# Kernel optimization log

Measured on AMD Instinct MI355X. Metric: run time of the kernel, lower is better.

The kernel has to match this reference:

```python
import jax, jax.numpy as jnp
import numpy as np

HEADS = 8
DH = 64          # value head dim == kernel head dim (expansion ratio 1.0)
DIM = 256
BOT = 256        # bottleneck_dim
DOUT = 256
HID = 4 * 256    # MLP hidden (expansion_ratio=4)
EPS_LN = 1e-5
EPS_GN = 1e-6


def layer_norm(x, g, b):
    m = x.mean(axis=-1, keepdims=True)
    v = x.var(axis=-1, keepdims=True)
    return (x - m) / jnp.sqrt(v + EPS_LN) * g + b


def rotate_half(x):
    x1, x2 = jnp.split(x, 2, axis=-1)
    return jnp.concatenate([-x2, x1], axis=-1)


def apply_rope(t, cos, sin):
    return t * cos + rotate_half(t) * sin


def mlp(x, W1, b1, W2, b2):
    return jax.nn.gelu(x @ W1 + b1) @ W2 + b2


def pooling_reducer(x, Win, W1, b1, W2, b2):
    # x: (b, n, m, c); mean-pool over axis 2, then MLP
    x = x @ Win
    x = x.mean(axis=2)
    return mlp(x, W1, b1, W2, b2)


def dp_kernel(x, Wqk, cos, sin):
    # x: (b, n, BOT) -> softmax attention kernel (b, h, n, n)
    b, n, _ = x.shape
    qk = (x @ Wqk).reshape(b, n, 2, HEADS, DH).transpose(0, 3, 2, 1, 4)  # b h 2 n d
    qk = apply_rope(qk, cos, sin)
    q, k = qk[:, :, 0], qk[:, :, 1]
    attn = jnp.einsum('bhid,bhjd->bhij', q, k) * (1.0 / DH)  # softmax scale = 1/dim_head
    return jax.nn.softmax(attn, axis=-1)


def group_norm(x):
    # channels-last GroupNorm(heads groups, affine=False), per position
    b, i, l, _ = x.shape
    xg = x.reshape(b, i, l, HEADS, DH)
    m = xg.mean(axis=-1, keepdims=True)
    v = xg.var(axis=-1, keepdims=True)
    return ((xg - m) / jnp.sqrt(v + EPS_GN)).reshape(b, i, l, HEADS * DH)


def setup_inputs() -> dict:
    key = jax.random.key(0)
    ks = jax.random.split(key, 32)
    B, NY, NX = 4, 128, 128
    s = 0.02
    d = {
        'u': jax.random.normal(ks[0], (B, NY, NX, DIM), jnp.float32),
        'rotary_cos_y': jax.random.uniform(ks[1], (NY, DH), jnp.float32),
        'rotary_sin_y': jax.random.uniform(ks[2], (NY, DH), jnp.float32),
        'rotary_cos_x': jax.random.uniform(ks[3], (NX, DH), jnp.float32),
        'rotary_sin_x': jax.random.uniform(ks[4], (NX, DH), jnp.float32),
        'scalar_cond': jax.random.normal(ks[5], (B,), jnp.float32),
        # norms
        'ln1_g': jnp.ones((DIM,), jnp.float32), 'ln1_b': jnp.zeros((DIM,), jnp.float32),
        'ln2_g': jnp.ones((DIM,), jnp.float32), 'ln2_b': jnp.zeros((DIM,), jnp.float32),
        # to_v
        'Wv': jax.random.normal(ks[6], (DIM, HEADS * DH), jnp.float32) * s,
        # to_y PoolingReducer
        'Wy_in': jax.random.normal(ks[7], (DIM, DIM), jnp.float32) * s,
        'Wy1': jax.random.normal(ks[8], (DIM, HID), jnp.float32) * s,
        'by1': jnp.zeros((HID,), jnp.float32),
        'Wy2': jax.random.normal(ks[9], (HID, BOT), jnp.float32) * s,
        'by2': jnp.zeros((BOT,), jnp.float32),
        # to_x PoolingReducer
        'Wx_in': jax.random.normal(ks[10], (DIM, DIM), jnp.float32) * s,
        'Wx1': jax.random.normal(ks[11], (DIM, HID), jnp.float32) * s,
        'bx1': jnp.zeros((HID,), jnp.float32),
        'Wx2': jax.random.normal(ks[12], (HID, BOT), jnp.float32) * s,
        'bx2': jnp.zeros((BOT,), jnp.float32),
        # kernels
        'Wqk_x': jax.random.normal(ks[13], (BOT, 2 * HEADS * DH), jnp.float32) * s,
        'Wqk_y': jax.random.normal(ks[14], (BOT, 2 * HEADS * DH), jnp.float32) * s,
        # merge head
        'Wm': jax.random.normal(ks[15], (HEADS * DH, DOUT), jnp.float32) * s,
        'bm': jnp.zeros((DOUT,), jnp.float32),
        # ffn
        'Wf1': jax.random.normal(ks[16], (DOUT, 4 * DOUT), jnp.float32) * s,
        'bf1': jnp.zeros((4 * DOUT,), jnp.float32),
        'Wf2': jax.random.normal(ks[17], (4 * DOUT, DOUT), jnp.float32) * s,
        'bf2': jnp.zeros((DOUT,), jnp.float32),
    }
    return d


def reference(u, rotary_cos_y, rotary_sin_y, rotary_cos_x, rotary_sin_x, scalar_cond,
              ln1_g, ln1_b, ln2_g, ln2_b, Wv,
              Wy_in, Wy1, by1, Wy2, by2,
              Wx_in, Wx1, bx1, Wx2, bx2,
              Wqk_x, Wqk_y, Wm, bm, Wf1, bf1, Wf2, bf2):
    b, ny, nx, _ = u.shape
    u_skip = u
    un = layer_norm(u, ln1_g, ln1_b)
    # to_x: transpose grid then pool over (now) second spatial axis -> (b, nx, BOT)
    u_x = pooling_reducer(un.transpose(0, 2, 1, 3), Wx_in, Wx1, bx1, Wx2, bx2)
    # to_y: pool over nx -> (b, ny, BOT)
    u_y = pooling_reducer(un, Wy_in, Wy1, by1, Wy2, by2)
    k_x = dp_kernel(u_x, Wqk_x, rotary_cos_x, rotary_sin_x)  # (b,h,nx,nx)
    k_y = dp_kernel(u_y, Wqk_y, rotary_cos_y, rotary_sin_y)  # (b,h,ny,ny)
    # values: b i l (h c) -> b h i l c
    v = (un @ Wv).reshape(b, ny, nx, HEADS, DH).transpose(0, 3, 1, 2, 4)
    u_phi = jnp.einsum('bhij,bhjmc->bhimc', k_y, v)
    u_phi = jnp.einsum('bhlm,bhimc->bhilc', k_x, u_phi)
    u_phi = u_phi.transpose(0, 2, 3, 1, 4).reshape(b, ny, nx, HEADS * DH)
    u2 = group_norm(u_phi) @ Wm + bm + u_skip  # dropout is identity in eval
    out = mlp(layer_norm(u2, ln2_g, ln2_b), Wf1, bf1, Wf2, bf2) + u2
    return out
```

## Files before the change

### kernel.cpp

```cpp
#include <hip/hip_runtime.h>
#include <hip/hip_bf16.h>
#include <math.h>

#define NB 4
#define NY 128
#define NX 128
#define DIM 256
#define NH 8
#define DH_ 64
#define HDIM 512
#define HID 1024
#define NPOS (NB*NY*NX)

typedef __hip_bfloat16 bf16_t;
typedef __attribute__((ext_vector_type(8))) short short8;
typedef __attribute__((ext_vector_type(4))) float f32x4;

__device__ __forceinline__ float b2f(bf16_t x){ return __bfloat162float(x); }
__device__ __forceinline__ bf16_t f2b(float x){ return __float2bfloat16(x); }
__device__ __forceinline__ short f2s(float x){ bf16_t h = __float2bfloat16(x); return *reinterpret_cast<short*>(&h); }
__device__ __forceinline__ float s2f(short x){ bf16_t h = *reinterpret_cast<bf16_t*>(&x); return __bfloat162float(h); }


__device__ __forceinline__ float gelu_tanh(float x){
  float z = 1.5957691216057308f*(x + 0.044715f*x*x*x);
  return x / (1.0f + __expf(-z));
}

__global__ void __launch_bounds__(256) k_pack(const float* __restrict__ W,
    short* __restrict__ out, int K, int N){
  int tid = blockIdx.x*256 + threadIdx.x;
  int lane = tid & 63;
  int rem = tid >> 6;
  int ntiles = N >> 4;
  int nt = rem % ntiles, kb = rem / ntiles;
  int n = nt*16 + (lane & 15);
  int k0 = kb*32 + (lane>>4)*8;
  short8 v;
  #pragma unroll
  for (int j=0;j<8;j++) v[j] = f2s(W[(size_t)(k0+j)*N + n]);
  *(short8*)&out[(size_t)tid*8] = v;
}

__global__ void __launch_bounds__(256) k_ln1(const float* __restrict__ u,
    const float* __restrict__ g, const float* __restrict__ b,
    bf16_t* __restrict__ un){
  int wave = threadIdx.x >> 6, lane = threadIdx.x & 63;
  size_t row = (size_t)blockIdx.x*4 + wave;
  const float* x = u + row*DIM;
  float v[4]; float s=0.f, ss=0.f;
  #pragma unroll
  for (int j=0;j<4;j++){ float t = x[lane + j*64]; v[j]=t; s+=t; ss+=t*t; }
  #pragma unroll
  for (int off=32;off>0;off>>=1){ s += __shfl_down(s,off,64); ss += __shfl_down(ss,off,64); }
  s = __shfl(s,0,64); ss = __shfl(ss,0,64);
  float m = s*(1.0f/DIM);
  float var = ss*(1.0f/DIM) - m*m;
  float r = rsqrtf(var + 1e-5f);
  bf16_t* o = un + row*DIM;
  #pragma unroll
  for (int j=0;j<4;j++){
    int f = lane + j*64;
    o[f] = f2b((v[j]-m)*r*g[f] + b[f]);
  }
}

__global__ void __launch_bounds__(256) k_pool_y(const bf16_t* __restrict__ un, float* __restrict__ pooly){
  int by = blockIdx.x;
  int d = threadIdx.x;
  size_t base = (size_t)by*NX*DIM + d;
  float s = 0.f;
  for (int x=0;x<NX;x++) s += b2f(un[base + (size_t)x*DIM]);
  pooly[(size_t)by*DIM + d] = s*(1.0f/NX);
}
__global__ void __launch_bounds__(256) k_pool_x(const bf16_t* __restrict__ un, float* __restrict__ poolx){
  int bb = blockIdx.x / NX, x = blockIdx.x % NX;
  int d = threadIdx.x;
  size_t base = ((size_t)bb*NY*NX + x)*DIM + d;
  float s = 0.f;
  for (int y=0;y<NY;y++) s += b2f(un[base + (size_t)y*NX*DIM]);
  poolx[(size_t)blockIdx.x*DIM + d] = s*(1.0f/NY);
}

#define GS_STRIDE 72
__global__ void __launch_bounds__(256) k_gemm_mfma(const float* __restrict__ A,
    const short* __restrict__ WP, const float* __restrict__ bias,
    float* __restrict__ C, int N, int K, int dogelu){
  __shared__ __align__(16) short As[64*GS_STRIDE];
  int tid = threadIdx.x;
  int lane = tid & 63, w = tid >> 6;
  int am = lane & 15, aq = lane >> 4;
  int m0 = blockIdx.x*64;
  int nt0 = blockIdx.y*16;
  int ntiles = N >> 4;
  f32x4 o[4][4];
  #pragma unroll
  for (int mt=0;mt<4;mt++)
    #pragma unroll
    for (int nt=0;nt<4;nt++) o[mt][nt] = (f32x4){0.f,0.f,0.f,0.f};

  for (int kc=0; kc<K; kc+=64){
    #pragma unroll
    for (int it=0; it<4; it++){
      int q = tid + it*256;
      int r = q >> 4, c4 = q & 15;
      float4 v = *(const float4*)&A[(size_t)(m0+r)*K + kc + c4*4];
      ushort4 p;
      p.x = (ushort)f2s(v.x); p.y = (ushort)f2s(v.y);
      p.z = (ushort)f2s(v.z); p.w = (ushort)f2s(v.w);
      *(ushort4*)&As[r*GS_STRIDE + c4*4] = p;
    }
    __syncthreads();
    #pragma unroll
    for (int kb=0; kb<2; kb++){
      short8 a[4], bfr[4];
      #pragma unroll
      for (int mt=0;mt<4;mt++)
        a[mt] = *(const short8*)&As[(mt*16+am)*GS_STRIDE + kb*32 + aq*8];
      int kbg = (kc>>5) + kb;
      #pragma unroll
      for (int nt=0;nt<4;nt++){
        int ntg = nt0 + w*4 + nt;
        bfr[nt] = *(const short8*)&WP[(size_t)((kbg*ntiles + ntg)*64 + lane)*8];
      }
      #pragma unroll
      for (int mt=0;mt<4;mt++)
        #pragma unroll
        for (int nt=0;nt<4;nt++)
          o[mt][nt] = __builtin_amdgcn_mfma_f32_16x16x32_bf16(a[mt], bfr[nt], o[mt][nt], 0,0,0);
    }
    __syncthreads();
  }

  #pragma unroll
  for (int nt=0;nt<4;nt++){
    int col = (nt0 + w*4 + nt)*16 + am;
    float bv = bias ? bias[col] : 0.f;
    #pragma unroll
    for (int mt=0;mt<4;mt++){
      #pragma unroll
      for (int reg=0;reg<4;reg++){
        int row = m0 + mt*16 + aq*4 + reg;
        float val = o[mt][nt][reg] + bv;
        if (dogelu) val = gelu_tanh(val);
        C[(size_t)row*N + col] = val;
      }
    }
  }
}

__global__ void __launch_bounds__(256) k_rope(const float* __restrict__ qk,
    const float* __restrict__ cs, const float* __restrict__ sn,
    float* __restrict__ q, float* __restrict__ k){
  int idx = blockIdx.x*256 + threadIdx.x;
  int c = idx & 63;
  int h = (idx>>6) & 7;
  int p = (idx>>9) & 1;
  int n = (idx>>10) & 127;
  int bb = idx>>17;
  float t = qk[idx];
  float t2 = qk[(c<32) ? idx+32 : idx-32];
  if (c<32) t2 = -t2;
  float val = t*cs[n*64+c] + t2*sn[n*64+c];
  float* dst = p ? k : q;
  dst[(((size_t)bb*NH + h)*128 + n)*64 + c] = val;
}

__global__ void __launch_bounds__(128) k_attn(const float* __restrict__ q,
    const float* __restrict__ k, bf16_t* __restrict__ attn){
  int i = blockIdx.x & 127;
  int bh = blockIdx.x >> 7;
  __shared__ float qs[64];
  __shared__ float sm[128];
  int tid = threadIdx.x;
  const float* qrow = q + ((size_t)bh*128 + i)*64;
  if (tid < 64) qs[tid] = qrow[tid];
  __syncthreads();
  const float* krow = k + ((size_t)bh*128 + tid)*64;
  float dot = 0.f;
  for (int c=0;c<64;c++) dot += qs[c]*krow[c];
  dot *= (1.0f/64.0f);
  sm[tid] = dot;
  __syncthreads();
  float mx = -1e30f;
  for (int j=0;j<128;j++) mx = fmaxf(mx, sm[j]);
  __syncthreads();
  float e = expf(dot - mx);
  sm[tid] = e;
  __syncthreads();
  float s = 0.f;
  for (int j=0;j<128;j++) s += sm[j];
  attn[(size_t)blockIdx.x*128 + tid] = f2b(e/s);
}

#define AST 136
#define UST 72
#define VST 136
__global__ void __launch_bounds__(256) k_phi1m(const bf16_t* __restrict__ un,
    const short* __restrict__ WvP, const bf16_t* __restrict__ attn,
    bf16_t* __restrict__ phi){
  int m  = blockIdx.x & (NX-1);
  int bh = blockIdx.x >> 7;
  int b  = bh >> 3, h = bh & 7;
  __shared__ __align__(16) short At[128*AST];
  __shared__ __align__(16) short unc[128*UST];
  __shared__ __align__(16) short Vt[64*VST];
  int tid = threadIdx.x;
  int lane = tid & 63, w = tid >> 6;
  int am = lane & 15, aq = lane >> 4;

  {
    const ushort* ag = (const ushort*)attn + (size_t)bh*16384;
    #pragma unroll
    for (int it=0; it<16; it++){
      int q = tid + it*256;
      int i = q >> 5, j4 = q & 31;
      *(ushort4*)&At[i*AST + j4*4] = *(const ushort4*)(ag + i*128 + j4*4);
    }
  }

  f32x4 v[2][4];
  #pragma unroll
  for (int mt=0;mt<2;mt++)
    #pragma unroll
    for (int nt=0;nt<4;nt++) v[mt][nt] = (f32x4){0.f,0.f,0.f,0.f};
  const ushort* ug = (const ushort*)un;
  for (int kc=0; kc<4; kc++){
    #pragma unroll
    for (int it=0; it<8; it++){
      int q = tid + it*256;
      int y = q >> 4, c4 = q & 15;
      *(ushort4*)&unc[y*UST + c4*4] =
          *(const ushort4*)(ug + (((size_t)b*NY + y)*NX + m)*DIM + kc*64 + c4*4);
    }
    __syncthreads();
    #pragma unroll
    for (int kb=0; kb<2; kb++){
      short8 a2[2], bb[4];
      #pragma unroll
      for (int mt=0;mt<2;mt++)
        a2[mt] = *(const short8*)&unc[(w*32 + mt*16 + am)*UST + kb*32 + aq*8];
      int kbg = kc*2 + kb;
      #pragma unroll
      for (int nt=0;nt<4;nt++)
        bb[nt] = *(const short8*)&WvP[(size_t)((kbg*32 + (h*4+nt))*64 + lane)*8];
      #pragma unroll
      for (int mt=0;mt<2;mt++)
        #pragma unroll
        for (int nt=0;nt<4;nt++)
          v[mt][nt] = __builtin_amdgcn_mfma_f32_16x16x32_bf16(a2[mt], bb[nt], v[mt][nt], 0,0,0);
    }
    __syncthreads();
  }
  #pragma unroll
  for (int mt=0;mt<2;mt++)
    #pragma unroll
    for (int nt=0;nt<4;nt++){
      int c = nt*16 + am;
      int y0 = w*32 + mt*16 + aq*4;
      ushort4 pk;
      pk.x = (ushort)f2s(v[mt][nt][0]);
      pk.y = (ushort)f2s(v[mt][nt][1]);
      pk.z = (ushort)f2s(v[mt][nt][2]);
      pk.w = (ushort)f2s(v[mt][nt][3]);
      *(ushort4*)&Vt[c*VST + y0] = pk;
    }
  __syncthreads();

  f32x4 o[2][4];
  #pragma unroll
  for (int mt=0;mt<2;mt++)
    #pragma unroll
    for (int nt=0;nt<4;nt++) o[mt][nt] = (f32x4){0.f,0.f,0.f,0.f};
  #pragma unroll
  for (int kb=0; kb<4; kb++){
    short8 a2[2], bb[4];
    #pragma unroll
    for (int mt=0;mt<2;mt++)
      a2[mt] = *(const short8*)&At[(w*32 + mt*16 + am)*AST + kb*32 + aq*8];
    #pragma unroll
    for (int nt=0;nt<4;nt++)
      bb[nt] = *(const short8*)&Vt[(nt*16 + am)*VST + kb*32 + aq*8];
    #pragma unroll
    for (int mt=0;mt<2;mt++)
      #pragma unroll
      for (int nt=0;nt<4;nt++)
        o[mt][nt] = __builtin_amdgcn_mfma_f32_16x16x32_bf16(a2[mt], bb[nt], o[mt][nt], 0,0,0);
  }
  ushort* pg = (ushort*)phi + (size_t)bh*NY*NX*DH_ + (size_t)m*DH_;
  #pragma unroll
  for (int mt=0;mt<2;mt++)
    #pragma unroll
    for (int nt=0;nt<4;nt++)
      #pragma unroll
      for (int reg=0;reg<4;reg++){
        int i = w*32 + mt*16 + aq*4 + reg;
        int c = nt*16 + am;
        pg[(size_t)i*(NX*DH_) + c] = (ushort)f2s(o[mt][nt][reg]);
      }
}

__global__ void __launch_bounds__(256) k_phi2m(const bf16_t* __restrict__ attn,
    bf16_t* __restrict__ phi){
  int i  = blockIdx.x & (NY-1);
  int bh = blockIdx.x >> 7;
  __shared__ __align__(16) short Ax[128*AST];
  __shared__ __align__(16) short Pt[64*VST];
  int tid = threadIdx.x;
  int lane = tid & 63, w = tid >> 6;
  int am = lane & 15, aq = lane >> 4;

  {
    const ushort* ag = (const ushort*)attn + (size_t)bh*16384;
    #pragma unroll
    for (int it=0; it<16; it++){
      int q = tid + it*256;
      int r = q >> 5, j4 = q & 31;
      *(ushort4*)&Ax[r*AST + j4*4] = *(const ushort4*)(ag + r*128 + j4*4);
    }
  }
  ushort* pg = (ushort*)phi + (size_t)(bh*NY + i)*(NX*DH_);
  #pragma unroll
  for (int it=0; it<8; it++){
    int q = tid + it*256;
    int mm = q >> 4, c4 = q & 15;
    ushort4 v4 = *(const ushort4*)(pg + mm*DH_ + c4*4);
    Pt[(c4*4+0)*VST + mm] = v4.x;
    Pt[(c4*4+1)*VST + mm] = v4.y;
    Pt[(c4*4+2)*VST + mm] = v4.z;
    Pt[(c4*4+3)*VST + mm] = v4.w;
  }
  __syncthreads();

  f32x4 o[2][4];
  #pragma unroll
  for (int mt=0;mt<2;mt++)
    #pragma unroll
    for (int nt=0;nt<4;nt++) o[mt][nt] = (f32x4){0.f,0.f,0.f,0.f};
  #pragma unroll
  for (int kb=0; kb<4; kb++){
    short8 a2[2], bb[4];
    #pragma unroll
    for (int mt=0;mt<2;mt++)
      a2[mt] = *(const short8*)&Ax[(w*32 + mt*16 + am)*AST + kb*32 + aq*8];
    #pragma unroll
    for (int nt=0;nt<4;nt++)
      bb[nt] = *(const short8*)&Pt[(nt*16 + am)*VST + kb*32 + aq*8];
    #pragma unroll
    for (int mt=0;mt<2;mt++)
      #pragma unroll
      for (int nt=0;nt<4;nt++)
        o[mt][nt] = __builtin_amdgcn_mfma_f32_16x16x32_bf16(a2[mt], bb[nt], o[mt][nt], 0,0,0);
  }
  #pragma unroll
  for (int mt=0;mt<2;mt++)
    #pragma unroll
    for (int nt=0;nt<4;nt++)
      #pragma unroll
      for (int reg=0;reg<4;reg++){
        int l = w*32 + mt*16 + aq*4 + reg;
        int c = nt*16 + am;
        pg[(size_t)l*DH_ + c] = (ushort)f2s(o[mt][nt][reg]);
      }
}

#define GN_STRIDE 520
__global__ void __launch_bounds__(512) k_gn_wm(const bf16_t* __restrict__ phi,
    const short* __restrict__ WmP, const float* __restrict__ bm,
    const float* __restrict__ u, float* __restrict__ u2){
  __shared__ __align__(16) short X[64*GN_STRIDE];
  __shared__ float mean_s[512], rstd_s[512];
  int tid = threadIdx.x;
  int lane = tid & 63, w = tid >> 6;
  int wh = w >> 2, wl = w & 3;
  size_t p0 = (size_t)blockIdx.x*64;
  int b  = (int)(p0 >> 14);
  int y  = (int)((p0 >> 7) & 127);
  int x0 = (int)(p0 & 127);

  #pragma unroll
  for (int it=0; it<16; it++){
    int q = tid + it*512;
    int r = q >> 7, f4 = q & 127;
    int h = f4 >> 4, c4 = f4 & 15;
    const ushort* src = (const ushort*)phi +
        ((((size_t)b*NH + h)*NY + y)*NX + (x0 + r))*DH_ + c4*4;
    *(ushort4*)&X[r*GN_STRIDE + f4*4] = *(const ushort4*)src;
  }
  __syncthreads();
  {
    int g = tid;
    int r = g >> 3, h = g & 7;
    const short* base = &X[r*GN_STRIDE + h*64];
    float s=0.f, ss=0.f;
    #pragma unroll
    for (int i=0;i<16;i++){
      ushort4 v4 = *(const ushort4*)&base[i*4];
      float a = s2f((short)v4.x), bq = s2f((short)v4.y), cq = s2f((short)v4.z), d = s2f((short)v4.w);
      s += a+bq+cq+d; ss += a*a+bq*bq+cq*cq+d*d;
    }
    float mm = s*(1.0f/64.0f);
    float vv = ss*(1.0f/64.0f) - mm*mm;
    mean_s[g] = mm;
    rstd_s[g] = rsqrtf(vv + 1e-6f);
  }
  __syncthreads();
  #pragma unroll
  for (int it=0; it<16; it++){
    int q = tid + it*512;
    int r = q >> 7, f4 = q & 127;
    int h = f4 >> 4;
    float mm = mean_s[r*8 + h], rs = rstd_s[r*8 + h];
    short* ptr = &X[r*GN_STRIDE + f4*4];
    ushort4 v4 = *(ushort4*)ptr;
    v4.x = (ushort)f2s((s2f((short)v4.x)-mm)*rs);
    v4.y = (ushort)f2s((s2f((short)v4.y)-mm)*rs);
    v4.z = (ushort)f2s((s2f((short)v4.z)-mm)*rs);
    v4.w = (ushort)f2s((s2f((short)v4.w)-mm)*rs);
    *(ushort4*)ptr = v4;
  }
  __syncthreads();

  f32x4 o[2][4];
  #pragma unroll
  for (int mt=0;mt<2;mt++)
    #pragma unroll
    for (int nt=0;nt<4;nt++) o[mt][nt] = (f32x4){0.f,0.f,0.f,0.f};
  int am = lane & 15, aq = lane >> 4;
  for (int kb=0; kb<16; kb++){
    short8 a[2], bfr[4];
    #pragma unroll
    for (int mt=0;mt<2;mt++)
      a[mt] = *(const short8*)&X[(wh*32 + mt*16 + am)*GN_STRIDE + kb*32 + aq*8];
    #pragma unroll
    for (int nt=0;nt<4;nt++)
      bfr[nt] = *(const short8*)&WmP[(size_t)((kb*16 + (wl*4+nt))*64 + lane)*8];
    #pragma unroll
    for (int mt=0;mt<2;mt++)
      #pragma unroll
      for (int nt=0;nt<4;nt++)
        o[mt][nt] = __builtin_amdgcn_mfma_f32_16x16x32_bf16(a[mt], bfr[nt], o[mt][nt], 0,0,0);
  }
  #pragma unroll
  for (int nt=0;nt<4;nt++){
    int col = wl*64 + nt*16 + am;
    float bmv = bm[col];
    #pragma unroll
    for (int mt=0;mt<2;mt++){
      #pragma unroll
      for (int reg=0;reg<4;reg++){
        size_t p = p0 + wh*32 + mt*16 + aq*4 + reg;
        u2[p*DIM + col] = o[mt][nt][reg] + bmv + u[p*DIM + col];
      }
    }
  }
}

#define ML_STRIDE 264
__global__ void __launch_bounds__(512) k_mlp_out(float* u2,
    const float* __restrict__ g2, const float* __restrict__ b2,
    const short* __restrict__ Wf1P, const float* __restrict__ bf1,
    const short* __restrict__ Wf2P, const float* __restrict__ bf2){
  __shared__ __align__(16) short X[64*ML_STRIDE];
  __shared__ __align__(16) short H[64*ML_STRIDE];
  int tid = threadIdx.x;
  int lane = tid & 63, w = tid >> 6;
  int wh = w >> 2, wl = w & 3;
  size_t p0 = (size_t)blockIdx.x*64;

  float4 g4 = *(const float4*)&g2[lane*4];
  float4 bq4 = *(const float4*)&b2[lane*4];
  for (int rr=0; rr<8; rr++){
    int r = w*8 + rr;
    float4 v = *(const float4*)&u2[(p0 + r)*DIM + lane*4];
    float s = v.x+v.y+v.z+v.w;
    float ss = v.x*v.x+v.y*v.y+v.z*v.z+v.w*v.w;
    #pragma unroll
    for (int off=32;off>0;off>>=1){ s += __shfl_down(s,off,64); ss += __shfl_down(ss,off,64); }
    s = __shfl(s,0,64); ss = __shfl(ss,0,64);
    float m = s*(1.0f/DIM);
    float rstd = rsqrtf(ss*(1.0f/DIM) - m*m + 1e-5f);
    ushort4 xo;
    xo.x = (ushort)f2s((v.x-m)*rstd*g4.x + bq4.x);
    xo.y = (ushort)f2s((v.y-m)*rstd*g4.y + bq4.y);
    xo.z = (ushort)f2s((v.z-m)*rstd*g4.z + bq4.z);
    xo.w = (ushort)f2s((v.w-m)*rstd*g4.w + bq4.w);
    *(ushort4*)&X[r*ML_STRIDE + lane*4] = xo;
  }
  __syncthreads();

  int am = lane & 15, aq = lane >> 4;
  f32x4 o[2][4];
  #pragma unroll
  for (int mt=0;mt<2;mt++)
    #pragma unroll
    for (int nt=0;nt<4;nt++) o[mt][nt] = (f32x4){0.f,0.f,0.f,0.f};

  for (int nc=0; nc<4; nc++){
    f32x4 hacc[2][4];
    #pragma unroll
    for (int mt=0;mt<2;mt++)
      #pragma unroll
      for (int nt=0;nt<4;nt++) hacc[mt][nt] = (f32x4){0.f,0.f,0.f,0.f};
    for (int kb=0; kb<8; kb++){
      short8 a[2], bfr[4];
      #pragma unroll
      for (int mt=0;mt<2;mt++)
        a[mt] = *(const short8*)&X[(wh*32 + mt*16 + am)*ML_STRIDE + kb*32 + aq*8];
      #pragma unroll
      for (int nt=0;nt<4;nt++){
        int ntg = nc*16 + wl*4 + nt;
        bfr[nt] = *(const short8*)&Wf1P[(size_t)((kb*64 + ntg)*64 + lane)*8];
      }
      #pragma unroll
      for (int mt=0;mt<2;mt++)
        #pragma unroll
        for (int nt=0;nt<4;nt++)
          hacc[mt][nt] = __builtin_amdgcn_mfma_f32_16x16x32_bf16(a[mt], bfr[nt], hacc[mt][nt], 0,0,0);
    }
    #pragma unroll
    for (int nt=0;nt<4;nt++){
      int col_l = wl*64 + nt*16 + am;
      float bv = bf1[nc*256 + col_l];
      #pragma unroll
      for (int mt=0;mt<2;mt++){
        #pragma unroll
        for (int reg=0;reg<4;reg++){
          int row = wh*32 + mt*16 + aq*4 + reg;
          H[row*ML_STRIDE + col_l] = f2s(gelu_tanh(hacc[mt][nt][reg] + bv));
        }
      }
    }
    __syncthreads();
    for (int kb=0; kb<8; kb++){
      short8 a[2], bfr[4];
      #pragma unroll
      for (int mt=0;mt<2;mt++)
        a[mt] = *(const short8*)&H[(wh*32 + mt*16 + am)*ML_STRIDE + kb*32 + aq*8];
      int kbg = nc*8 + kb;
      #pragma unroll
      for (int nt=0;nt<4;nt++)
        bfr[nt] = *(const short8*)&Wf2P[(size_t)((kbg*16 + (wl*4+nt))*64 + lane)*8];
      #pragma unroll
      for (int mt=0;mt<2;mt++)
        #pragma unroll
        for (int nt=0;nt<4;nt++)
          o[mt][nt] = __builtin_amdgcn_mfma_f32_16x16x32_bf16(a[mt], bfr[nt], o[mt][nt], 0,0,0);
    }
    __syncthreads();
  }

  #pragma unroll
  for (int nt=0;nt<4;nt++){
    int col = wl*64 + nt*16 + am;
    float bv = bf2[col];
    #pragma unroll
    for (int mt=0;mt<2;mt++){
      #pragma unroll
      for (int reg=0;reg<4;reg++){
        size_t p = p0 + wh*32 + mt*16 + aq*4 + reg;
        float res = u2[p*DIM + col];
        u2[p*DIM + col] = o[mt][nt][reg] + bv + res;
      }
    }
  }
}

extern "C" void kernel_launch(void* const* d_in, const int* in_sizes, int n_in,
                              void* d_out, int out_size, void* d_ws, size_t ws_size,
                              hipStream_t stream){
  const float* u    = (const float*)d_in[0];
  const float* rcy  = (const float*)d_in[1];
  const float* rsy  = (const float*)d_in[2];
  const float* rcx  = (const float*)d_in[3];
  const float* rsx  = (const float*)d_in[4];
  const float* ln1g = (const float*)d_in[6];
  const float* ln1b = (const float*)d_in[7];
  const float* ln2g = (const float*)d_in[8];
  const float* ln2b = (const float*)d_in[9];
  const float* Wv   = (const float*)d_in[10];
  const float* Wyin = (const float*)d_in[11];
  const float* Wy1  = (const float*)d_in[12];
  const float* by1  = (const float*)d_in[13];
  const float* Wy2  = (const float*)d_in[14];
  const float* by2  = (const float*)d_in[15];
  const float* Wxin = (const float*)d_in[16];
  const float* Wx1  = (const float*)d_in[17];
  const float* bx1  = (const float*)d_in[18];
  const float* Wx2  = (const float*)d_in[19];
  const float* bx2  = (const float*)d_in[20];
  const float* Wqkx = (const float*)d_in[21];
  const float* Wqky = (const float*)d_in[22];
  const float* Wm   = (const float*)d_in[23];
  const float* bm   = (const float*)d_in[24];
  const float* Wf1  = (const float*)d_in[25];
  const float* bf1  = (const float*)d_in[26];
  const float* Wf2  = (const float*)d_in[27];
  const float* bf2  = (const float*)d_in[28];

  char* w = (char*)d_ws;
  auto alloc = [&](size_t n) -> void* {
    void* p = (void*)w;
    w += (n + 255) & ~(size_t)255;
    return p;
  };
  bf16_t* UN   = (bf16_t*)alloc((size_t)NPOS*DIM*2);
  bf16_t* PHI  = (bf16_t*)alloc((size_t)NB*NH*NY*NX*DH_*2);
  float* POOLY = (float*)alloc((size_t)NB*NY*DIM*4);
  float* POOLX = (float*)alloc((size_t)NB*NX*DIM*4);
  float* TY    = (float*)alloc((size_t)512*256*4);
  float* TX    = (float*)alloc((size_t)512*256*4);
  float* HY    = (float*)alloc((size_t)512*1024*4);
  float* HX    = (float*)alloc((size_t)512*1024*4);
  float* UY    = (float*)alloc((size_t)512*256*4);
  float* UX    = (float*)alloc((size_t)512*256*4);
  float* QKY   = (float*)alloc((size_t)512*1024*4);
  float* QKX   = (float*)alloc((size_t)512*1024*4);
  float* QRY   = (float*)alloc((size_t)NB*NH*128*64*4);
  float* KRY   = (float*)alloc((size_t)NB*NH*128*64*4);
  float* QRX   = (float*)alloc((size_t)NB*NH*128*64*4);
  float* KRX   = (float*)alloc((size_t)NB*NH*128*64*4);
  bf16_t* ATTNY = (bf16_t*)alloc((size_t)NB*NH*128*128*2);
  bf16_t* ATTNX = (bf16_t*)alloc((size_t)NB*NH*128*128*2);
  short* WF1P  = (short*)alloc((size_t)256*1024*2);
  short* WF2P  = (short*)alloc((size_t)1024*256*2);
  short* WMP   = (short*)alloc((size_t)512*256*2);
  short* WVP   = (short*)alloc((size_t)256*512*2);
  short* WYINP = (short*)alloc((size_t)256*256*2);
  short* WY1P  = (short*)alloc((size_t)256*1024*2);
  short* WY2P  = (short*)alloc((size_t)1024*256*2);
  short* WQKYP = (short*)alloc((size_t)256*1024*2);
  short* WXINP = (short*)alloc((size_t)256*256*2);
  short* WX1P  = (short*)alloc((size_t)256*1024*2);
  short* WX2P  = (short*)alloc((size_t)1024*256*2);
  short* WQKXP = (short*)alloc((size_t)256*1024*2);
  float* U2 = (float*)d_out;
  (void)in_sizes; (void)n_in; (void)out_size; (void)ws_size;

  k_pack<<<(256*1024/8)/256, 256, 0, stream>>>(Wf1, WF1P, 256, 1024);
  k_pack<<<(1024*256/8)/256, 256, 0, stream>>>(Wf2, WF2P, 1024, 256);
  k_pack<<<(512*256/8)/256, 256, 0, stream>>>(Wm, WMP, 512, 256);
  k_pack<<<(256*512/8)/256, 256, 0, stream>>>(Wv, WVP, 256, 512);
  k_pack<<<(256*256/8)/256, 256, 0, stream>>>(Wyin, WYINP, 256, 256);
  k_pack<<<(256*1024/8)/256, 256, 0, stream>>>(Wy1, WY1P, 256, 1024);
  k_pack<<<(1024*256/8)/256, 256, 0, stream>>>(Wy2, WY2P, 1024, 256);
  k_pack<<<(256*1024/8)/256, 256, 0, stream>>>(Wqky, WQKYP, 256, 1024);
  k_pack<<<(256*256/8)/256, 256, 0, stream>>>(Wxin, WXINP, 256, 256);
  k_pack<<<(256*1024/8)/256, 256, 0, stream>>>(Wx1, WX1P, 256, 1024);
  k_pack<<<(1024*256/8)/256, 256, 0, stream>>>(Wx2, WX2P, 1024, 256);
  k_pack<<<(256*1024/8)/256, 256, 0, stream>>>(Wqkx, WQKXP, 256, 1024);

  k_ln1<<<NPOS/4, 256, 0, stream>>>(u, ln1g, ln1b, UN);
  k_pool_y<<<NB*NY, 256, 0, stream>>>(UN, POOLY);
  k_pool_x<<<NB*NX, 256, 0, stream>>>(UN, POOLX);

  k_gemm_mfma<<<dim3(8,1), 256, 0, stream>>>(POOLY, WYINP, (const float*)nullptr, TY, 256, 256, 0);
  k_gemm_mfma<<<dim3(8,4), 256, 0, stream>>>(TY, WY1P, by1, HY, 1024, 256, 1);
  k_gemm_mfma<<<dim3(8,1), 256, 0, stream>>>(HY, WY2P, by2, UY, 256, 1024, 0);
  k_gemm_mfma<<<dim3(8,4), 256, 0, stream>>>(UY, WQKYP, (const float*)nullptr, QKY, 1024, 256, 0);
  k_gemm_mfma<<<dim3(8,1), 256, 0, stream>>>(POOLX, WXINP, (const float*)nullptr, TX, 256, 256, 0);
  k_gemm_mfma<<<dim3(8,4), 256, 0, stream>>>(TX, WX1P, bx1, HX, 1024, 256, 1);
  k_gemm_mfma<<<dim3(8,1), 256, 0, stream>>>(HX, WX2P, bx2, UX, 256, 1024, 0);
  k_gemm_mfma<<<dim3(8,4), 256, 0, stream>>>(UX, WQKXP, (const float*)nullptr, QKX, 1024, 256, 0);

  k_rope<<<(NB*128*1024)/256, 256, 0, stream>>>(QKY, rcy, rsy, QRY, KRY);
  k_rope<<<(NB*128*1024)/256, 256, 0, stream>>>(QKX, rcx, rsx, QRX, KRX);
  k_attn<<<NB*NH*128, 128, 0, stream>>>(QRY, KRY, ATTNY);
  k_attn<<<NB*NH*128, 128, 0, stream>>>(QRX, KRX, ATTNX);
  k_phi1m<<<NB*NH*NX, 256, 0, stream>>>(UN, WVP, ATTNY, PHI);
  k_phi2m<<<NB*NH*NY, 256, 0, stream>>>(ATTNX, PHI);
  k_gn_wm<<<NPOS/64, 512, 0, stream>>>(PHI, WMP, bm, u, U2);
  k_mlp_out<<<NPOS/64, 512, 0, stream>>>(U2, ln2g, ln2b, WF1P, bf1, WF2P, bf2);
}
```

Before: 679.2 us.

## Fuse GroupNorm+Wm projection with LayerNorm MLP tail and batch x/y small GEMMs

Merges the GroupNorm/Wm projection kernel and the LN2+MLP kernel into one k_tail kernel. The intermediate u2 stays in registers, LN2 statistics come from a cross-wave shuffle and shared-memory reduction, and the residual is folded into the accumulator init. This removes a full fp32 write and read of u2 across all positions. Separately, the y and x pooling-reducer GEMM chains are batched into one launch each via blockIdx.z, halving the small-GEMM launches. The fused kernel holds more live registers and uses a launch_bounds occupancy hint, which could cause register pressure.

```diff
diff --git a/kernel.cpp b/kernel.cpp
--- a/kernel.cpp
+++ b/kernel.cpp
@@ -83,9 +83,15 @@
 }
 
 #define GS_STRIDE 72
-__global__ void __launch_bounds__(256) k_gemm_mfma(const float* __restrict__ A,
-    const short* __restrict__ WP, const float* __restrict__ bias,
-    float* __restrict__ C, int N, int K, int dogelu){
+__global__ void __launch_bounds__(256) k_gemm2(const float* __restrict__ A0,
+    const float* __restrict__ A1,
+    const short* __restrict__ W0, const short* __restrict__ W1,
+    const float* __restrict__ b0, const float* __restrict__ b1,
+    float* __restrict__ C0, float* __restrict__ C1, int N, int K, int dogelu){
+  const float* A  = blockIdx.z ? A1 : A0;
+  const short* WP = blockIdx.z ? W1 : W0;
+  const float* bias = blockIdx.z ? b1 : b0;
+  float* C = blockIdx.z ? C1 : C0;
   __shared__ __align__(16) short As[64*GS_STRIDE];
   int tid = threadIdx.x;
   int lane = tid & 63, w = tid >> 6;
@@ -364,15 +370,26 @@
       }
 }
 
-#define GN_STRIDE 520
-__global__ void __launch_bounds__(512) k_gn_wm(const bf16_t* __restrict__ phi,
+#define GN_ST 520
+#define ML_ST 264
+__global__ void __launch_bounds__(512, 4) k_tail(const bf16_t* __restrict__ phi,
     const short* __restrict__ WmP, const float* __restrict__ bm,
-    const float* __restrict__ u, float* __restrict__ u2){
-  __shared__ __align__(16) short X[64*GN_STRIDE];
+    const float* __restrict__ u,
+    const float* __restrict__ g2, const float* __restrict__ b2,
+    const short* __restrict__ Wf1P, const float* __restrict__ bf1,
+    const short* __restrict__ Wf2P, const float* __restrict__ bf2,
+    float* __restrict__ out){
+  __shared__ __align__(16) short SMEM[64*ML_ST*2];
   __shared__ float mean_s[512], rstd_s[512];
+  __shared__ float prow[64][4], prow2[64][4];
+  __shared__ float mrow[64], rrow[64];
+  short* Xg = SMEM;
+  short* Xm = SMEM;
+  short* H  = SMEM + 64*ML_ST;
   int tid = threadIdx.x;
   int lane = tid & 63, w = tid >> 6;
   int wh = w >> 2, wl = w & 3;
+  int am = lane & 15, aq = lane >> 4;
   size_t p0 = (size_t)blockIdx.x*64;
   int b  = (int)(p0 >> 14);
   int y  = (int)((p0 >> 7) & 127);
@@ -385,13 +402,13 @@
     int h = f4 >> 4, c4 = f4 & 15;
     const ushort* src = (const ushort*)phi +
         ((((size_t)b*NH + h)*NY + y)*NX + (x0 + r))*DH_ + c4*4;
-    *(ushort4*)&X[r*GN_STRIDE + f4*4] = *(const ushort4*)src;
+    *(ushort4*)&Xg[r*GN_ST + f4*4] = *(const ushort4*)src;
   }
   __syncthreads();
   {
     int g = tid;
     int r = g >> 3, h = g & 7;
-    const short* base = &X[r*GN_STRIDE + h*64];
+    const short* base = &Xg[r*GN_ST + h*64];
     float s=0.f, ss=0.f;
     #pragma unroll
     for (int i=0;i<16;i++){
@@ -411,7 +428,7 @@
     int r = q >> 7, f4 = q & 127;
     int h = f4 >> 4;
     float mm = mean_s[r*8 + h], rs = rstd_s[r*8 + h];
-    short* ptr = &X[r*GN_STRIDE + f4*4];
+    short* ptr = &Xg[r*GN_ST + f4*4];
     ushort4 v4 = *(ushort4*)ptr;
     v4.x = (ushort)f2s((s2f((short)v4.x)-mm)*rs);
     v4.y = (ushort)f2s((s2f((short)v4.y)-mm)*rs);
@@ -421,17 +438,16 @@
   }
   __syncthreads();
 
-  f32x4 o[2][4];
-  #pragma unroll
-  for (int mt=0;mt<2;mt++)
-    #pragma unroll
-    for (int nt=0;nt<4;nt++) o[mt][nt] = (f32x4){0.f,0.f,0.f,0.f};
-  int am = lane & 15, aq = lane >> 4;
+  f32x4 u2r[2][4];
+  #pragma unroll
+  for (int mt=0;mt<2;mt++)
+    #pragma unroll
+    for (int nt=0;nt<4;nt++) u2r[mt][nt] = (f32x4){0.f,0.f,0.f,0.f};
   for (int kb=0; kb<16; kb++){
     short8 a[2], bfr[4];
     #pragma unroll
     for (int mt=0;mt<2;mt++)
-      a[mt] = *(const short8*)&X[(wh*32 + mt*16 + am)*GN_STRIDE + kb*32 + aq*8];
+      a[mt] = *(const short8*)&Xg[(wh*32 + mt*16 + am)*GN_ST + kb*32 + aq*8];
     #pragma unroll
     for (int nt=0;nt<4;nt++)
       bfr[nt] = *(const short8*)&WmP[(size_t)((kb*16 + (wl*4+nt))*64 + lane)*8];
@@ -439,7 +455,7 @@
     for (int mt=0;mt<2;mt++)
       #pragma unroll
       for (int nt=0;nt<4;nt++)
-        o[mt][nt] = __builtin_amdgcn_mfma_f32_16x16x32_bf16(a[mt], bfr[nt], o[mt][nt], 0,0,0);
+        u2r[mt][nt] = __builtin_amdgcn_mfma_f32_16x16x32_bf16(a[mt], bfr[nt], u2r[mt][nt], 0,0,0);
   }
   #pragma unroll
   for (int nt=0;nt<4;nt++){
@@ -450,51 +466,59 @@
       #pragma unroll
       for (int reg=0;reg<4;reg++){
         size_t p = p0 + wh*32 + mt*16 + aq*4 + reg;
-        u2[p*DIM + col] = o[mt][nt][reg] + bmv + u[p*DIM + col];
-      }
-    }
-  }
-}
-
-#define ML_STRIDE 264
-__global__ void __launch_bounds__(512) k_mlp_out(float* u2,
-    const float* __restrict__ g2, const float* __restrict__ b2,
-    const short* __restrict__ Wf1P, const float* __restrict__ bf1,
-    const short* __restrict__ Wf2P, const float* __restrict__ bf2){
-  __shared__ __align__(16) short X[64*ML_STRIDE];
-  __shared__ __align__(16) short H[64*ML_STRIDE];
-  int tid = threadIdx.x;
-  int lane = tid & 63, w = tid >> 6;
-  int wh = w >> 2, wl = w & 3;
-  size_t p0 = (size_t)blockIdx.x*64;
-
-  float4 g4 = *(const float4*)&g2[lane*4];
-  float4 bq4 = *(const float4*)&b2[lane*4];
-  for (int rr=0; rr<8; rr++){
-    int r = w*8 + rr;
-    float4 v = *(const float4*)&u2[(p0 + r)*DIM + lane*4];
-    float s = v.x+v.y+v.z+v.w;
-    float ss = v.x*v.x+v.y*v.y+v.z*v.z+v.w*v.w;
-    #pragma unroll
-    for (int off=32;off>0;off>>=1){ s += __shfl_down(s,off,64); ss += __shfl_down(ss,off,64); }
-    s = __shfl(s,0,64); ss = __shfl(ss,0,64);
+        u2r[mt][nt][reg] += bmv + u[p*DIM + col];
+      }
+    }
+  }
+
+  #pragma unroll
+  for (int mt=0;mt<2;mt++){
+    #pragma unroll
+    for (int reg=0;reg<4;reg++){
+      float s  = u2r[mt][0][reg]+u2r[mt][1][reg]+u2r[mt][2][reg]+u2r[mt][3][reg];
+      float ss = u2r[mt][0][reg]*u2r[mt][0][reg]+u2r[mt][1][reg]*u2r[mt][1][reg]
+               + u2r[mt][2][reg]*u2r[mt][2][reg]+u2r[mt][3][reg]*u2r[mt][3][reg];
+      #pragma unroll
+      for (int msk=1; msk<16; msk<<=1){
+        s  += __shfl_xor(s,  msk, 64);
+        ss += __shfl_xor(ss, msk, 64);
+      }
+      if (am == 0){
+        int r = wh*32 + mt*16 + aq*4 + reg;
+        prow[r][wl] = s;
+        prow2[r][wl] = ss;
+      }
+    }
+  }
+  __syncthreads();
+  if (tid < 64){
+    float s  = prow[tid][0]+prow[tid][1]+prow[tid][2]+prow[tid][3];
+    float ss = prow2[tid][0]+prow2[tid][1]+prow2[tid][2]+prow2[tid][3];
     float m = s*(1.0f/DIM);
-    float rstd = rsqrtf(ss*(1.0f/DIM) - m*m + 1e-5f);
-    ushort4 xo;
-    xo.x = (ushort)f2s((v.x-m)*rstd*g4.x + bq4.x);
-    xo.y = (ushort)f2s((v.y-m)*rstd*g4.y + bq4.y);
-    xo.z = (ushort)f2s((v.z-m)*rstd*g4.z + bq4.z);
-    xo.w = (ushort)f2s((v.w-m)*rstd*g4.w + bq4.w);
-    *(ushort4*)&X[r*ML_STRIDE + lane*4] = xo;
-  }
-  __syncthreads();
-
-  int am = lane & 15, aq = lane >> 4;
-  f32x4 o[2][4];
-  #pragma unroll
-  for (int mt=0;mt<2;mt++)
-    #pragma unroll
-    for (int nt=0;nt<4;nt++) o[mt][nt] = (f32x4){0.f,0.f,0.f,0.f};
+    mrow[tid] = m;
+    rrow[tid] = rsqrtf(ss*(1.0f/DIM) - m*m + 1e-5f);
+  }
+  __syncthreads();
+  #pragma unroll
+  for (int nt=0;nt<4;nt++){
+    int col = wl*64 + nt*16 + am;
+    float gg = g2[col], bb2 = b2[col];
+    #pragma unroll
+    for (int mt=0;mt<2;mt++){
+      #pragma unroll
+      for (int reg=0;reg<4;reg++){
+        int r = wh*32 + mt*16 + aq*4 + reg;
+        Xm[r*ML_ST + col] = f2s((u2r[mt][nt][reg]-mrow[r])*rrow[r]*gg + bb2);
+      }
+    }
+  }
+  __syncthreads();
+
+  f32x4 o2[2][4];
+  #pragma unroll
+  for (int mt=0;mt<2;mt++)
+    #pragma unroll
+    for (int nt=0;nt<4;nt++) o2[mt][nt] = u2r[mt][nt];
 
   for (int nc=0; nc<4; nc++){
     f32x4 hacc[2][4];
@@ -506,7 +530,7 @@
       short8 a[2], bfr[4];
       #pragma unroll
       for (int mt=0;mt<2;mt++)
-        a[mt] = *(const short8*)&X[(wh*32 + mt*16 + am)*ML_STRIDE + kb*32 + aq*8];
+        a[mt] = *(const short8*)&Xm[(wh*32 + mt*16 + am)*ML_ST + kb*32 + aq*8];
       #pragma unroll
       for (int nt=0;nt<4;nt++){
         int ntg = nc*16 + wl*4 + nt;
@@ -527,7 +551,7 @@
         #pragma unroll
         for (int reg=0;reg<4;reg++){
           int row = wh*32 + mt*16 + aq*4 + reg;
-          H[row*ML_STRIDE + col_l] = f2s(gelu_tanh(hacc[mt][nt][reg] + bv));
+          H[row*ML_ST + col_l] = f2s(gelu_tanh(hacc[mt][nt][reg] + bv));
         }
       }
     }
@@ -536,7 +560,7 @@
       short8 a[2], bfr[4];
       #pragma unroll
       for (int mt=0;mt<2;mt++)
-        a[mt] = *(const short8*)&H[(wh*32 + mt*16 + am)*ML_STRIDE + kb*32 + aq*8];
+        a[mt] = *(const short8*)&H[(wh*32 + mt*16 + am)*ML_ST + kb*32 + aq*8];
       int kbg = nc*8 + kb;
       #pragma unroll
       for (int nt=0;nt<4;nt++)
@@ -545,7 +569,7 @@
       for (int mt=0;mt<2;mt++)
         #pragma unroll
         for (int nt=0;nt<4;nt++)
-          o[mt][nt] = __builtin_amdgcn_mfma_f32_16x16x32_bf16(a[mt], bfr[nt], o[mt][nt], 0,0,0);
+          o2[mt][nt] = __builtin_amdgcn_mfma_f32_16x16x32_bf16(a[mt], bfr[nt], o2[mt][nt], 0,0,0);
     }
     __syncthreads();
   }
@@ -559,8 +583,7 @@
       #pragma unroll
       for (int reg=0;reg<4;reg++){
         size_t p = p0 + wh*32 + mt*16 + aq*4 + reg;
-        float res = u2[p*DIM + col];
-        u2[p*DIM + col] = o[mt][nt][reg] + bv + res;
+        out[p*DIM + col] = o2[mt][nt][reg] + bv;
       }
     }
   }
@@ -654,14 +677,12 @@
   k_pool_y<<<NB*NY, 256, 0, stream>>>(UN, POOLY);
   k_pool_x<<<NB*NX, 256, 0, stream>>>(UN, POOLX);
 
-  k_gemm_mfma<<<dim3(8,1), 256, 0, stream>>>(POOLY, WYINP, (const float*)nullptr, TY, 256, 256, 0);
-  k_gemm_mfma<<<dim3(8,4), 256, 0, stream>>>(TY, WY1P, by1, HY, 1024, 256, 1);
-  k_gemm_mfma<<<dim3(8,1), 256, 0, stream>>>(HY, WY2P, by2, UY, 256, 1024, 0);
-  k_gemm_mfma<<<dim3(8,4), 256, 0, stream>>>(UY, WQKYP, (const float*)nullptr, QKY, 1024, 256, 0);
-  k_gemm_mfma<<<dim3(8,1), 256, 0, stream>>>(POOLX, WXINP, (const float*)nullptr, TX, 256, 256, 0);
-  k_gemm_mfma<<<dim3(8,4), 256, 0, stream>>>(TX, WX1P, bx1, HX, 1024, 256, 1);
-  k_gemm_mfma<<<dim3(8,1), 256, 0, stream>>>(HX, WX2P, bx2, UX, 256, 1024, 0);
-  k_gemm_mfma<<<dim3(8,4), 256, 0, stream>>>(UX, WQKXP, (const float*)nullptr, QKX, 1024, 256, 0);
+  k_gemm2<<<dim3(8,1,2), 256, 0, stream>>>(POOLY, POOLX, WYINP, WXINP,
+      (const float*)nullptr, (const float*)nullptr, TY, TX, 256, 256, 0);
+  k_gemm2<<<dim3(8,4,2), 256, 0, stream>>>(TY, TX, WY1P, WX1P, by1, bx1, HY, HX, 1024, 256, 1);
+  k_gemm2<<<dim3(8,1,2), 256, 0, stream>>>(HY, HX, WY2P, WX2P, by2, bx2, UY, UX, 256, 1024, 0);
+  k_gemm2<<<dim3(8,4,2), 256, 0, stream>>>(UY, UX, WQKYP, WQKXP,
+      (const float*)nullptr, (const float*)nullptr, QKY, QKX, 1024, 256, 0);
 
   k_rope<<<(NB*128*1024)/256, 256, 0, stream>>>(QKY, rcy, rsy, QRY, KRY);
   k_rope<<<(NB*128*1024)/256, 256, 0, stream>>>(QKX, rcx, rsx, QRX, KRX);
@@ -669,6 +690,6 @@
   k_attn<<<NB*NH*128, 128, 0, stream>>>(QRX, KRX, ATTNX);
   k_phi1m<<<NB*NH*NX, 256, 0, stream>>>(UN, WVP, ATTNY, PHI);
   k_phi2m<<<NB*NH*NY, 256, 0, stream>>>(ATTNX, PHI);
-  k_gn_wm<<<NPOS/64, 512, 0, stream>>>(PHI, WMP, bm, u, U2);
-  k_mlp_out<<<NPOS/64, 512, 0, stream>>>(U2, ln2g, ln2b, WF1P, bf1, WF2P, bf2);
-}
+  k_tail<<<NPOS/64, 512, 0, stream>>>(PHI, WMP, bm, u, ln2g, ln2b,
+      WF1P, bf1, WF2P, bf2, U2);
+}
```

Result: faster. 610.5 us (-10.1%).
